# Kernel tuning notes

Hardware: AMD Instinct MI355X
Metric: run time of the kernel (lower is better)

The kernel has to match this reference:

```python
import jax, jax.numpy as jnp
import numpy as np

SQRT_2_OVER_PI = float(np.sqrt(2.0 / np.pi))
EPS = 1e-5
EPS_VAR = 1e-4
NORM_EPS = 1e-12  # F.normalize default


def _gelu_tanh(x):
    return 0.5 * x * (1.0 + jnp.tanh(SQRT_2_OVER_PI * (x + 0.044715 * x ** 3)))


def setup_inputs() -> dict:
    key = jax.random.key(0)
    k1, k2, k3, k4 = jax.random.split(key, 4)
    B, T, D = 4, 4096, 2048
    x = jax.random.normal(k1, (B, T, D), dtype=jnp.float32)
    ema_mean = 0.1 * jax.random.normal(k2, (D,), dtype=jnp.float32)
    # ensure ema_sq - ema_mean^2 > 0 so variance clamp is realistic
    ema_sq = ema_mean ** 2 + jax.random.uniform(k3, (D,), dtype=jnp.float32, minval=0.5, maxval=1.5)
    ema_out = jax.random.normal(k4, (D,), dtype=jnp.float32)
    return {
        "x": x,
        "ema_mean": ema_mean,
        "ema_sq": ema_sq,
        "ema_out": ema_out,
        "surp_ema": jnp.float32(0.05),
        "log_tau": jnp.float32(np.log(2.0)),
        "log_sigma": jnp.float32(np.log(np.exp(0.3) - 1.0)),
        "log_w_raw": jnp.float32(np.log(np.exp(1.0) - 1.0)),
    }


def reference(x, ema_mean, ema_sq, ema_out, surp_ema, log_tau, log_sigma, log_w_raw):
    # learned scalar transforms (differentiable)
    tau = jnp.exp(log_tau)
    sigma = jax.nn.softplus(log_sigma)
    w = jax.nn.softplus(log_w_raw)

    out = _gelu_tanh(x)  # [B,T,D]

    # --- surprise score: z-score vs EMA stats (all detached in torch) ---
    xd = jax.lax.stop_gradient(x)
    mu = jax.lax.stop_gradient(ema_mean)                     # [D]
    var = jnp.maximum(jax.lax.stop_gradient(ema_sq) - mu ** 2, EPS_VAR)
    std = jnp.sqrt(var)                                      # [D]
    z = (xd - mu) / (std + EPS)                               # [B,T,D]
    mean_absz = jnp.mean(jnp.abs(z), axis=-1)                 # [B,T]

    surp_raw = jnp.tanh(sigma * mean_absz)                    # grad flows only via sigma
    surp_mod = jax.nn.relu(surp_raw - jax.lax.stop_gradient(surp_ema))

    # --- cosine similarity of detached output vs EMA direction ---
    outd = jax.lax.stop_gradient(out)
    out_n = outd / jnp.maximum(jnp.linalg.norm(outd, axis=-1, keepdims=True), NORM_EPS)
    eo = jax.lax.stop_gradient(ema_out)
    ema_n = eo / jnp.maximum(jnp.linalg.norm(eo), NORM_EPS)   # [D]
    cos_sim = jnp.clip(jnp.sum(out_n * ema_n, axis=-1), -1.0, 1.0)  # [B,T]

    gate = jnp.exp(-tau * cos_sim) * (1.0 + w * surp_mod)     # [B,T]
    return out * gate[..., None]
```

## Files before the change

### kernel.cpp

```cpp
#include <hip/hip_runtime.h>
#include <math.h>

#define D 2048
#define NTHREADS 256
#define VEC_PER_THREAD 2


__global__ __launch_bounds__(NTHREADS) void precompute_kernel(
    const float* __restrict__ ema_mean,
    const float* __restrict__ ema_sq,
    const float* __restrict__ ema_out,
    const float* __restrict__ surp_ema,
    const float* __restrict__ log_tau,
    const float* __restrict__ log_sigma,
    const float* __restrict__ log_w_raw,
    float* __restrict__ ws) {
  const int t = threadIdx.x;
  float eo2 = 0.f;
#pragma unroll
  for (int i = 0; i < D / NTHREADS; ++i) {
    const int d = t + i * NTHREADS;
    const float mu = ema_mean[d];
    const float var = fmaxf(ema_sq[d] - mu * mu, 1e-4f);
    ws[d] = 1.0f / (sqrtf(var) + 1e-5f);
    const float e = ema_out[d];
    eo2 += e * e;
  }
  __shared__ float s[4];
#pragma unroll
  for (int off = 32; off > 0; off >>= 1) eo2 += __shfl_down(eo2, off);
  if ((t & 63) == 0) s[t >> 6] = eo2;
  __syncthreads();
  if (t == 0) {
    const float norm_e = sqrtf(s[0] + s[1] + s[2] + s[3]);
    ws[D + 0] = expf(log_tau[0]);
    ws[D + 1] = log1pf(expf(log_sigma[0]));
    ws[D + 2] = log1pf(expf(log_w_raw[0]));
    ws[D + 3] = surp_ema[0];
    ws[D + 4] = 1.0f / fmaxf(norm_e, 1e-12f);
  }
}

__global__ __launch_bounds__(NTHREADS) void gate_kernel(
    const float* __restrict__ x,
    const float* __restrict__ ema_mean,
    const float* __restrict__ ema_out,
    const float* __restrict__ ws,
    float* __restrict__ out) {
  const int row = blockIdx.x;
  const int t = threadIdx.x;
  const float* __restrict__ xr = x + (size_t)row * D;
  float* __restrict__ outr = out + (size_t)row * D;

  const float tau    = ws[D + 0];
  const float sigma  = ws[D + 1];
  const float w      = ws[D + 2];
  const float surp_e = ws[D + 3];
  const float inv_ne = ws[D + 4];

  const float kC = 0.7978845608028654f;

  float o[VEC_PER_THREAD * 4];
  float sum_absz = 0.f, sum_o2 = 0.f, sum_dot = 0.f;

#pragma unroll
  for (int i = 0; i < VEC_PER_THREAD; ++i) {
    const int v = t + i * NTHREADS;
    const float4 xv = ((const float4*)xr)[v];
    const float4 mv = ((const float4*)ema_mean)[v];
    const float4 iv = ((const float4*)ws)[v];
    const float4 ev = ((const float4*)ema_out)[v];
    const float xs[4] = {xv.x, xv.y, xv.z, xv.w};
    const float ms[4] = {mv.x, mv.y, mv.z, mv.w};
    const float is[4] = {iv.x, iv.y, iv.z, iv.w};
    const float es[4] = {ev.x, ev.y, ev.z, ev.w};
#pragma unroll
    for (int j = 0; j < 4; ++j) {
      const float xx = xs[j];
      const float inner = kC * (xx + 0.044715f * xx * xx * xx);
      const float g = 0.5f * xx * (1.0f + tanhf(inner));
      o[i * 4 + j] = g;
      sum_absz += fabsf((xx - ms[j]) * is[j]);
      sum_o2   += g * g;
      sum_dot  += g * es[j];
    }
  }

#pragma unroll
  for (int off = 32; off > 0; off >>= 1) {
    sum_absz += __shfl_down(sum_absz, off);
    sum_o2   += __shfl_down(sum_o2, off);
    sum_dot  += __shfl_down(sum_dot, off);
  }
  __shared__ float sred[3][4];
  const int wave = t >> 6;
  if ((t & 63) == 0) {
    sred[0][wave] = sum_absz;
    sred[1][wave] = sum_o2;
    sred[2][wave] = sum_dot;
  }
  __syncthreads();
  const float tot_absz = sred[0][0] + sred[0][1] + sred[0][2] + sred[0][3];
  const float tot_o2   = sred[1][0] + sred[1][1] + sred[1][2] + sred[1][3];
  const float tot_dot  = sred[2][0] + sred[2][1] + sred[2][2] + sred[2][3];

  const float mean_absz = tot_absz * (1.0f / (float)D);
  const float surp_raw  = tanhf(sigma * mean_absz);
  const float surp_mod  = fmaxf(surp_raw - surp_e, 0.0f);
  const float inv_no    = 1.0f / fmaxf(sqrtf(tot_o2), 1e-12f);
  float cs = tot_dot * inv_no * inv_ne;
  cs = fminf(fmaxf(cs, -1.0f), 1.0f);
  const float gate = expf(-tau * cs) * (1.0f + w * surp_mod);

#pragma unroll
  for (int i = 0; i < VEC_PER_THREAD; ++i) {
    const int v = t + i * NTHREADS;
    float4 r;
    r.x = o[i * 4 + 0] * gate;
    r.y = o[i * 4 + 1] * gate;
    r.z = o[i * 4 + 2] * gate;
    r.w = o[i * 4 + 3] * gate;
    ((float4*)outr)[v] = r;
  }
}

extern "C" void kernel_launch(void* const* d_in, const int* in_sizes, int n_in,
                              void* d_out, int out_size, void* d_ws, size_t ws_size,
                              hipStream_t stream) {
  const float* x        = (const float*)d_in[0];
  const float* ema_mean = (const float*)d_in[1];
  const float* ema_sq   = (const float*)d_in[2];
  const float* ema_out  = (const float*)d_in[3];
  const float* surp_ema = (const float*)d_in[4];
  const float* log_tau  = (const float*)d_in[5];
  const float* log_sig  = (const float*)d_in[6];
  const float* log_wr   = (const float*)d_in[7];
  float* out = (float*)d_out;
  float* ws  = (float*)d_ws;

  const int rows = in_sizes[0] / D;

  precompute_kernel<<<1, NTHREADS, 0, stream>>>(
      ema_mean, ema_sq, ema_out, surp_ema, log_tau, log_sig, log_wr, ws);
  gate_kernel<<<rows, NTHREADS, 0, stream>>>(x, ema_mean, ema_out, ws, out);
}
```

Before: 247.6 us.

## Fuse precompute into gate kernel with fast-math GELU and nontemporal memory ops

Removes the separate single-block precompute kernel. Per-channel inverse std, the ema_out norm and the scalar transforms are now recomputed inside each row block. GELU-tanh is rewritten as x*sigmoid form using __expf and hardware reciprocal, and rsq intrinsics replace sqrt/divide. x loads and out stores use nontemporal hints. This trades redundant per-block work and slight precision changes (e.g. the +1e-5 std epsilon is dropped) for one fewer launch and less ALU cost.

Result: no change. 244.7 us (-1.2%).

```diff
diff --git a/kernel.cpp b/kernel.cpp
--- a/kernel.cpp
+++ b/kernel.cpp
@@ -2,11 +2,12 @@
 #include <math.h>
 
 #define D 2048
-#define NTHREADS 256
-#define VEC_PER_THREAD 2
+#define NT 256
 
+typedef float floatx4 __attribute__((ext_vector_type(4)));
 
-__global__ __launch_bounds__(NTHREADS) void precompute_kernel(
+__global__ __launch_bounds__(NT) void fused_gate_kernel(
+    const float* __restrict__ x,
     const float* __restrict__ ema_mean,
     const float* __restrict__ ema_sq,
     const float* __restrict__ ema_out,
@@ -14,113 +15,87 @@
     const float* __restrict__ log_tau,
     const float* __restrict__ log_sigma,
     const float* __restrict__ log_w_raw,
-    float* __restrict__ ws) {
-  const int t = threadIdx.x;
-  float eo2 = 0.f;
-#pragma unroll
-  for (int i = 0; i < D / NTHREADS; ++i) {
-    const int d = t + i * NTHREADS;
-    const float mu = ema_mean[d];
-    const float var = fmaxf(ema_sq[d] - mu * mu, 1e-4f);
-    ws[d] = 1.0f / (sqrtf(var) + 1e-5f);
-    const float e = ema_out[d];
-    eo2 += e * e;
-  }
-  __shared__ float s[4];
-#pragma unroll
-  for (int off = 32; off > 0; off >>= 1) eo2 += __shfl_down(eo2, off);
-  if ((t & 63) == 0) s[t >> 6] = eo2;
-  __syncthreads();
-  if (t == 0) {
-    const float norm_e = sqrtf(s[0] + s[1] + s[2] + s[3]);
-    ws[D + 0] = expf(log_tau[0]);
-    ws[D + 1] = log1pf(expf(log_sigma[0]));
-    ws[D + 2] = log1pf(expf(log_w_raw[0]));
-    ws[D + 3] = surp_ema[0];
-    ws[D + 4] = 1.0f / fmaxf(norm_e, 1e-12f);
-  }
-}
-
-__global__ __launch_bounds__(NTHREADS) void gate_kernel(
-    const float* __restrict__ x,
-    const float* __restrict__ ema_mean,
-    const float* __restrict__ ema_out,
-    const float* __restrict__ ws,
     float* __restrict__ out) {
   const int row = blockIdx.x;
   const int t = threadIdx.x;
   const float* __restrict__ xr = x + (size_t)row * D;
   float* __restrict__ outr = out + (size_t)row * D;
 
-  const float tau    = ws[D + 0];
-  const float sigma  = ws[D + 1];
-  const float w      = ws[D + 2];
-  const float surp_e = ws[D + 3];
-  const float inv_ne = ws[D + 4];
+  const float tau    = __expf(log_tau[0]);
+  const float sigma  = log1pf(__expf(log_sigma[0]));
+  const float w      = log1pf(__expf(log_w_raw[0]));
+  const float surp_e = surp_ema[0];
 
-  const float kC = 0.7978845608028654f;
+  const float c1 = -2.0f * 0.7978845608028654f;
+  const float c2 = c1 * 0.044715f;
 
-  float o[VEC_PER_THREAD * 4];
-  float sum_absz = 0.f, sum_o2 = 0.f, sum_dot = 0.f;
+  float o[8];
+  float s_absz = 0.f, s_o2 = 0.f, s_dot = 0.f, s_e2 = 0.f;
 
 #pragma unroll
-  for (int i = 0; i < VEC_PER_THREAD; ++i) {
-    const int v = t + i * NTHREADS;
-    const float4 xv = ((const float4*)xr)[v];
-    const float4 mv = ((const float4*)ema_mean)[v];
-    const float4 iv = ((const float4*)ws)[v];
-    const float4 ev = ((const float4*)ema_out)[v];
-    const float xs[4] = {xv.x, xv.y, xv.z, xv.w};
-    const float ms[4] = {mv.x, mv.y, mv.z, mv.w};
-    const float is[4] = {iv.x, iv.y, iv.z, iv.w};
-    const float es[4] = {ev.x, ev.y, ev.z, ev.w};
+  for (int i = 0; i < 2; ++i) {
+    const int v = t + i * NT;
+    const floatx4 xv = __builtin_nontemporal_load((const floatx4*)xr + v);
+    const floatx4 mv = ((const floatx4*)ema_mean)[v];
+    const floatx4 qv = ((const floatx4*)ema_sq)[v];
+    const floatx4 ev = ((const floatx4*)ema_out)[v];
 #pragma unroll
     for (int j = 0; j < 4; ++j) {
-      const float xx = xs[j];
-      const float inner = kC * (xx + 0.044715f * xx * xx * xx);
-      const float g = 0.5f * xx * (1.0f + tanhf(inner));
+      const float xx = xv[j];
+      const float x2 = xx * xx;
+      const float u2 = xx * fmaf(c2, x2, c1);
+      const float g  = xx * __builtin_amdgcn_rcpf(1.0f + __expf(u2));
       o[i * 4 + j] = g;
-      sum_absz += fabsf((xx - ms[j]) * is[j]);
-      sum_o2   += g * g;
-      sum_dot  += g * es[j];
+      const float mu  = mv[j];
+      const float var = fmaxf(fmaf(-mu, mu, qv[j]), 1e-4f);
+      const float inv = __builtin_amdgcn_rsqf(var);
+      s_absz += fabsf((xx - mu) * inv);
+      const float e = ev[j];
+      s_o2  = fmaf(g, g, s_o2);
+      s_dot = fmaf(g, e, s_dot);
+      s_e2  = fmaf(e, e, s_e2);
     }
   }
 
 #pragma unroll
   for (int off = 32; off > 0; off >>= 1) {
-    sum_absz += __shfl_down(sum_absz, off);
-    sum_o2   += __shfl_down(sum_o2, off);
-    sum_dot  += __shfl_down(sum_dot, off);
+    s_absz += __shfl_down(s_absz, off);
+    s_o2   += __shfl_down(s_o2, off);
+    s_dot  += __shfl_down(s_dot, off);
+    s_e2   += __shfl_down(s_e2, off);
   }
-  __shared__ float sred[3][4];
+  __shared__ float sred[4][4];
   const int wave = t >> 6;
   if ((t & 63) == 0) {
-    sred[0][wave] = sum_absz;
-    sred[1][wave] = sum_o2;
-    sred[2][wave] = sum_dot;
+    sred[0][wave] = s_absz;
+    sred[1][wave] = s_o2;
+    sred[2][wave] = s_dot;
+    sred[3][wave] = s_e2;
   }
   __syncthreads();
   const float tot_absz = sred[0][0] + sred[0][1] + sred[0][2] + sred[0][3];
   const float tot_o2   = sred[1][0] + sred[1][1] + sred[1][2] + sred[1][3];
   const float tot_dot  = sred[2][0] + sred[2][1] + sred[2][2] + sred[2][3];
+  const float tot_e2   = sred[3][0] + sred[3][1] + sred[3][2] + sred[3][3];
 
   const float mean_absz = tot_absz * (1.0f / (float)D);
   const float surp_raw  = tanhf(sigma * mean_absz);
   const float surp_mod  = fmaxf(surp_raw - surp_e, 0.0f);
-  const float inv_no    = 1.0f / fmaxf(sqrtf(tot_o2), 1e-12f);
+  const float inv_no = __builtin_amdgcn_rsqf(fmaxf(tot_o2, 1e-24f));
+  const float inv_ne = __builtin_amdgcn_rsqf(fmaxf(tot_e2, 1e-24f));
   float cs = tot_dot * inv_no * inv_ne;
   cs = fminf(fmaxf(cs, -1.0f), 1.0f);
-  const float gate = expf(-tau * cs) * (1.0f + w * surp_mod);
+  const float gate = __expf(-tau * cs) * (1.0f + w * surp_mod);
 
 #pragma unroll
-  for (int i = 0; i < VEC_PER_THREAD; ++i) {
-    const int v = t + i * NTHREADS;
-    float4 r;
-    r.x = o[i * 4 + 0] * gate;
-    r.y = o[i * 4 + 1] * gate;
-    r.z = o[i * 4 + 2] * gate;
-    r.w = o[i * 4 + 3] * gate;
-    ((float4*)outr)[v] = r;
+  for (int i = 0; i < 2; ++i) {
+    const int v = t + i * NT;
+    floatx4 r;
+    r[0] = o[i * 4 + 0] * gate;
+    r[1] = o[i * 4 + 1] * gate;
+    r[2] = o[i * 4 + 2] * gate;
+    r[3] = o[i * 4 + 3] * gate;
+    __builtin_nontemporal_store(r, (floatx4*)outr + v);
   }
 }
 
@@ -136,11 +111,9 @@
   const float* log_sig  = (const float*)d_in[6];
   const float* log_wr   = (const float*)d_in[7];
   float* out = (float*)d_out;
-  float* ws  = (float*)d_ws;
 
   const int rows = in_sizes[0] / D;
 
-  precompute_kernel<<<1, NTHREADS, 0, stream>>>(
-      ema_mean, ema_sq, ema_out, surp_ema, log_tau, log_sig, log_wr, ws);
-  gate_kernel<<<rows, NTHREADS, 0, stream>>>(x, ema_mean, ema_out, ws, out);
+  fused_gate_kernel<<<rows, NT, 0, stream>>>(
+      x, ema_mean, ema_sq, ema_out, surp_ema, log_tau, log_sig, log_wr, out);
 }
```
